# Performance work log

Measured on AMD Instinct MI355X. Metric: run time of the kernel, lower is better.

The kernel has to match this reference:

```python
import jax, jax.numpy as jnp
import numpy as np

EPS_BN = 1e-5

def _conv1x1(x, w, b):
    # x: [B,C,N], w: [O,C], b: [O] -> [B,O,N]
    return jnp.einsum('oc,bcn->bon', w, x) + b[:, None]

def _bn(x, g, b):
    # BatchNorm1d in training mode: batch stats over (B, N), biased variance
    mu = jnp.mean(x, axis=(0, 2), keepdims=True)
    var = jnp.var(x, axis=(0, 2), keepdims=True)
    return g[:, None] * (x - mu) / jnp.sqrt(var + EPS_BN) + b[:, None]

def _lrelu(x):
    return jnp.where(x >= 0, x, 0.2 * x)

def setup_inputs() -> dict:
    key = jax.random.key(0)
    B, N, S = 4, 16384, 2048
    D1, D2, FINT = 128, 256, 64
    IN, M1, M2 = D1 + D2, 256, 128
    ks = jax.random.split(key, 20)
    def rn(k, shape, scale=1.0):
        return jax.random.normal(k, shape, dtype=jnp.float32) * scale
    return {
        'xyz1': rn(ks[0], (B, 3, N)),
        'xyz2': rn(ks[1], (B, 3, S)),
        'points1': rn(ks[2], (B, D1, N)),
        'points2': rn(ks[3], (B, D2, S)),
        'conv1_w': rn(ks[4], (M1, IN), 0.05), 'conv1_b': rn(ks[5], (M1,), 0.05),
        'bn1_g': jnp.ones((M1,), jnp.float32), 'bn1_b': jnp.zeros((M1,), jnp.float32),
        'conv2_w': rn(ks[6], (M2, M1), 0.05), 'conv2_b': rn(ks[7], (M2,), 0.05),
        'bn2_g': jnp.ones((M2,), jnp.float32), 'bn2_b': jnp.zeros((M2,), jnp.float32),
        'wg_w': rn(ks[8], (FINT, D2), 0.05), 'wg_b': rn(ks[9], (FINT,), 0.05),
        'wg_bn_g': jnp.ones((FINT,), jnp.float32), 'wg_bn_b': jnp.zeros((FINT,), jnp.float32),
        'wx_w': rn(ks[10], (FINT, D1), 0.05), 'wx_b': rn(ks[11], (FINT,), 0.05),
        'wx_bn_g': jnp.ones((FINT,), jnp.float32), 'wx_bn_b': jnp.zeros((FINT,), jnp.float32),
        'psi_w': rn(ks[12], (1, FINT), 0.05), 'psi_b': rn(ks[13], (1,), 0.05),
        'psi_bn_g': jnp.ones((1,), jnp.float32), 'psi_bn_b': jnp.zeros((1,), jnp.float32),
    }

def reference(xyz1, xyz2, points1, points2,
              conv1_w, conv1_b, bn1_g, bn1_b,
              conv2_w, conv2_b, bn2_g, bn2_b,
              wg_w, wg_b, wg_bn_g, wg_bn_b,
              wx_w, wx_b, wx_bn_g, wx_bn_b,
              psi_w, psi_b, psi_bn_g, psi_bn_b):
    x1 = xyz1.transpose(0, 2, 1)        # [B,N,3]
    x2 = xyz2.transpose(0, 2, 1)        # [B,S,3]
    p2 = points2.transpose(0, 2, 1)     # [B,S,D2]
    # squared euclidean distances [B,N,S]
    d = (jnp.sum(x1 * x1, -1)[:, :, None]
         + jnp.sum(x2 * x2, -1)[:, None, :]
         - 2.0 * jnp.einsum('bnc,bsc->bns', x1, x2))
    # 3 smallest distances (torch: full sort + slice [:3])
    neg, idx = jax.lax.top_k(-d, 3)     # idx: [B,N,3]
    d3 = -neg
    recip = 1.0 / (d3 + 1e-8)
    w = recip / jnp.sum(recip, -1, keepdims=True)  # [B,N,3]
    gathered = jax.vmap(lambda p, i: p[i])(p2, idx)  # [B,N,3,D2]
    interp = jnp.einsum('bnkd,bnk->bnd', gathered, w)  # [B,N,D2]
    interp_t = interp.transpose(0, 2, 1)               # [B,D2,N]
    # attention gate: g = interpolated, x = points1
    g1 = _bn(_conv1x1(interp_t, wg_w, wg_b), wg_bn_g, wg_bn_b)
    xx1 = _bn(_conv1x1(points1, wx_w, wx_b), wx_bn_g, wx_bn_b)
    psi = jax.nn.sigmoid(_bn(_conv1x1(_lrelu(g1 + xx1), psi_w, psi_b), psi_bn_g, psi_bn_b))
    p1 = points1 * psi                                  # [B,D1,N]
    new = jnp.concatenate([p1, interp_t], axis=1)       # [B,D1+D2,N]
    new = _lrelu(_bn(_conv1x1(new, conv1_w, conv1_b), bn1_g, bn1_b))
    new = _lrelu(_bn(_conv1x1(new, conv2_w, conv2_b), bn2_g, bn2_b))
    return new
```

## Files before the change

### kernel.cpp

```cpp
#include <hip/hip_runtime.h>
#include <hip/hip_bf16.h>

#define Bq    4
#define NPTS  16384
#define SPTS  2048
#define NCH   8
#define SCH   (SPTS/NCH)
#define CNTF  65536.0f
#define BNEPS 1e-5f

typedef unsigned short u16t;
typedef unsigned int   u32t;
typedef __attribute__((ext_vector_type(8))) short s16x8;
typedef __attribute__((ext_vector_type(4))) float f32x4;

#define AS1(p) ((const __attribute__((address_space(1))) void*)(p))
#define AS3(p) ((__attribute__((address_space(3))) void*)(p))

__device__ __forceinline__ float b2f(u16t u){
  union { u32t i; float f; } v; v.i = ((u32t)u) << 16; return v.f;
}
__device__ __forceinline__ u16t f2b(float f){
  __hip_bfloat16 h = __float2bfloat16(f);
  return *reinterpret_cast<u16t*>(&h);
}
__device__ __forceinline__ float lrelu(float x){ return x >= 0.0f ? x : 0.2f*x; }

#define ST_WG  0
#define ST_WX  128
#define ST_PSI 256
#define ST_BN1 272
#define ST_BN2 784

#define WOFF_C1 0
#define WOFF_C2 98304
#define WOFF_WG 131072
#define WOFF_WX 147456
#define WTOTAL  155648

#define O_STATS  0u
#define O_WB     8192u
#define O_PSIPRE 319488u
#define O_SP     O_PSIPRE
#define O_P2T    581632u
#define O_PART   O_P2T
#define O_P1T    4775936u
#define O_INT    21553152u
#define O_H1     55107584u
#define O_PD     O_H1
#define O_PI     (O_H1 + 6291456u)
#define O_IDX3   (O_H1 + 12582912u)
#define O_W3     (O_H1 + 13369344u)
#define O_YG     O_H1
#define O_YX     (O_H1 + 8388608u)
#define O_H2     O_INT

__global__ __launch_bounds__(256) void knn_prep_kernel(const float* __restrict__ xyz2, float4* __restrict__ sp){
  int i = blockIdx.x*256 + threadIdx.x;
  int b = i >> 11, s = i & (SPTS-1);
  float x = xyz2[(b*3+0)*SPTS+s];
  float y = xyz2[(b*3+1)*SPTS+s];
  float z = xyz2[(b*3+2)*SPTS+s];
  sp[i] = make_float4(x, y, z, x*x+y*y+z*z);
}

__global__ __launch_bounds__(256) void knn_part_kernel(const float* __restrict__ xyz1, const float4* __restrict__ sp,
                                                       float* __restrict__ pd, int* __restrict__ pi){
  const int b = blockIdx.z;
  const int c = blockIdx.y;
  const int n = blockIdx.x*256 + threadIdx.x;
  const float4* cp = sp + (size_t)b*SPTS + c*SCH;
  float px = xyz1[(b*3+0)*NPTS+n];
  float py = xyz1[(b*3+1)*NPTS+n];
  float pz = xyz1[(b*3+2)*NPTS+n];
  float s1 = px*px+py*py+pz*pz;
  float d0=3.4e38f, d1=3.4e38f, d2=3.4e38f;
  int   i0=0, i1=0, i2=0;
  const int cbase = c*SCH;
  #pragma unroll 8
  for (int s=0; s<SCH; ++s){
    float4 q = cp[s];
    float dot = fmaf(pz, q.z, fmaf(py, q.y, px*q.x));
    float key = (s1 + q.w) - 2.0f*dot;
    int gi = cbase + s;
    bool c0 = key < d0, c1 = key < d1, c2 = key < d2;
    int ni2 = c1 ? i1 : (c2 ? gi : i2);
    int ni1 = c0 ? i0 : (c1 ? gi : i1);
    i0 = c0 ? gi : i0;
    float nd2 = fminf(d2, fmaxf(d1, key));
    d1 = __builtin_amdgcn_fmed3f(d0, d1, key);
    d0 = fminf(d0, key);
    d2 = nd2; i1 = ni1; i2 = ni2;
  }
  size_t base = (((size_t)b*NPTS + n)*NCH + c)*3;
  pd[base]=d0; pd[base+1]=d1; pd[base+2]=d2;
  pi[base]=i0; pi[base+1]=i1; pi[base+2]=i2;
}

__global__ __launch_bounds__(256) void knn_merge_kernel(const float* __restrict__ pd, const int* __restrict__ pi,
                                                        int* __restrict__ idx3, float* __restrict__ w3){
  const int p = blockIdx.x*256 + threadIdx.x;
  const float* dp = pd + (size_t)p*NCH*3;
  const int*   ip = pi + (size_t)p*NCH*3;
  float d0=3.4e38f, d1=3.4e38f, d2=3.4e38f;
  int   i0=0, i1=0, i2=0;
  #pragma unroll
  for (int k=0; k<NCH*3; ++k){
    float key = dp[k]; int gi = ip[k];
    bool c0 = key < d0, c1 = key < d1, c2 = key < d2;
    int ni2 = c1 ? i1 : (c2 ? gi : i2);
    int ni1 = c0 ? i0 : (c1 ? gi : i1);
    i0 = c0 ? gi : i0;
    float nd2 = fminf(d2, fmaxf(d1, key));
    d1 = __builtin_amdgcn_fmed3f(d0, d1, key);
    d0 = fminf(d0, key);
    d2 = nd2; i1 = ni1; i2 = ni2;
  }
  float r0=1.0f/(d0+1e-8f), r1=1.0f/(d1+1e-8f), r2=1.0f/(d2+1e-8f);
  float rs = r0+r1+r2;
  size_t base = (size_t)p*3;
  idx3[base]=i0; idx3[base+1]=i1; idx3[base+2]=i2;
  w3[base]=r0/rs; w3[base+1]=r1/rs; w3[base+2]=r2/rs;
}

template<int C, int NN>
__global__ __launch_bounds__(256) void tpose_kernel(const float* __restrict__ src, u16t* __restrict__ dst){
  __shared__ float tile[64][65];
  const int n0 = blockIdx.x * 64;
  const int c0 = blockIdx.y * 64;
  const int b  = blockIdx.z;
  const int t  = threadIdx.x;
  #pragma unroll
  for (int i = 0; i < 16; ++i){
    int idx = t + i*256;
    int cc = idx >> 6, nn = idx & 63;
    tile[cc][nn] = src[((size_t)b*C + c0 + cc)*NN + n0 + nn];
  }
  __syncthreads();
  #pragma unroll
  for (int i = 0; i < 16; ++i){
    int idx = t + i*256;
    int nn = idx >> 6, cc = idx & 63;
    dst[((size_t)b*NN + n0 + nn)*C + c0 + cc] = f2b(tile[cc][nn]);
  }
}

__global__ __launch_bounds__(256) void wcvt_kernel(const float* __restrict__ w1, const float* __restrict__ w2,
                                                   const float* __restrict__ wg, const float* __restrict__ wx,
                                                   u16t* __restrict__ wb){
  int i = blockIdx.x*256 + threadIdx.x;
  if (i >= WTOTAL) return;
  float v;
  if      (i < WOFF_C2) v = w1[i];
  else if (i < WOFF_WG) v = w2[i - WOFF_C2];
  else if (i < WOFF_WX) v = wg[i - WOFF_WG];
  else                  v = wx[i - WOFF_WX];
  wb[i] = f2b(v);
}

__global__ __launch_bounds__(256) void interp_kernel(const u16t* __restrict__ p2t, const int* __restrict__ idx3,
                                                     const float* __restrict__ w3, u16t* __restrict__ it){
  const int t = threadIdx.x;
  const int pid = blockIdx.x*8 + (t >> 5);
  const int l = t & 31;
  const int b = pid >> 14;
  size_t pb = (size_t)pid*3;
  int i0 = idx3[pb], i1 = idx3[pb+1], i2 = idx3[pb+2];
  float w0 = w3[pb], w1 = w3[pb+1], w2 = w3[pb+2];
  const u16t* r0 = p2t + ((size_t)b*SPTS + i0)*256 + l*8;
  const u16t* r1 = p2t + ((size_t)b*SPTS + i1)*256 + l*8;
  const u16t* r2 = p2t + ((size_t)b*SPTS + i2)*256 + l*8;
  uint4 q0 = *reinterpret_cast<const uint4*>(r0);
  uint4 q1 = *reinterpret_cast<const uint4*>(r1);
  uint4 q2 = *reinterpret_cast<const uint4*>(r2);
  const u32t* a0 = reinterpret_cast<const u32t*>(&q0);
  const u32t* a1 = reinterpret_cast<const u32t*>(&q1);
  const u32t* a2 = reinterpret_cast<const u32t*>(&q2);
  u32t ow[4];
  #pragma unroll
  for (int j = 0; j < 4; ++j){
    u32t u0 = a0[j], u1 = a1[j], u2 = a2[j];
    float lo = fmaf(w2, b2f((u16t)u2), fmaf(w1, b2f((u16t)u1), w0*b2f((u16t)u0)));
    float hi = fmaf(w2, b2f((u16t)(u2>>16)), fmaf(w1, b2f((u16t)(u1>>16)), w0*b2f((u16t)(u0>>16))));
    ow[j] = (u32t)f2b(lo) | ((u32t)f2b(hi) << 16);
  }
  *reinterpret_cast<uint4*>(it + (size_t)pid*256 + l*8) = make_uint4(ow[0], ow[1], ow[2], ow[3]);
}

template<int CIN, int OUT, bool SPLIT>
__global__ __launch_bounds__(256, 1) void mfma_conv_kernel(const u16t* __restrict__ xa, const u16t* __restrict__ xb,
                                                           const u16t* __restrict__ W, const float* __restrict__ bias,
                                                           u16t* __restrict__ y, float* __restrict__ partial,
                                                           const float* __restrict__ psipre, const float* __restrict__ stpsi,
                                                           const float* __restrict__ pbn_g, const float* __restrict__ pbn_b){
  constexpr int MW = OUT/4;
  constexpr int MF = MW/16;
  constexpr int NC = CIN/64;
  constexpr int CSTR = OUT + 8;
  constexpr int LDSZ = (CSTR*64 > 8192) ? CSTR*64 : 8192;
  __shared__ u16t lds[LDSZ];
  u16t* sbuf0 = lds;
  u16t* sbuf1 = lds + 4096;
  const int bid = blockIdx.x;
  const int b = bid >> 8;
  const int n0 = (bid & 255) * 64;
  const int wv = threadIdx.x >> 6;
  const int lane = threadIdx.x & 63;
  const int lr = lane & 15;
  const int kg = lane >> 4;
  const int m0 = wv * MW;
  const int t = threadIdx.x;

  float psiv[4];
  if (SPLIT){
    float m  = stpsi[0]*(1.0f/CNTF);
    float vv = fmaxf(stpsi[1]*(1.0f/CNTF) - m*m, 0.0f);
    float iv = 1.0f/sqrtf(vv + BNEPS);
    float ap = pbn_g[0]*iv;
    float bp = pbn_b[0] - m*ap;
    #pragma unroll
    for (int nf = 0; nf < 4; ++nf){
      float z = fmaf(psipre[b*NPTS + n0 + nf*16 + lr], ap, bp);
      psiv[nf] = 1.0f/(1.0f + expf(-z));
    }
  }

  f32x4 acc[MF][4];
  #pragma unroll
  for (int mf = 0; mf < MF; ++mf)
    #pragma unroll
    for (int nf = 0; nf < 4; ++nf){ acc[mf][nf][0]=0.f; acc[mf][nf][1]=0.f; acc[mf][nf][2]=0.f; acc[mf][nf][3]=0.f; }

  const u16t* wrow[MF];
  #pragma unroll
  for (int mf = 0; mf < MF; ++mf)
    wrow[mf] = W + (size_t)(m0 + mf*16 + lr)*CIN + kg*8;

  const int prow0 = wv*16 + (lane>>3);
  const int gslot = (lane & 7) ^ ((lane >> 3) & 7);
  int rdoff[2][4];
  #pragma unroll
  for (int ks = 0; ks < 2; ++ks)
    #pragma unroll
    for (int nf = 0; nf < 4; ++nf)
      rdoff[ks][nf] = (nf*16 + lr)*64 + (((ks*4 + kg) ^ (lr & 7)) << 3);

  auto stage = [&](int c, int buf){
    #pragma unroll
    for (int i = 0; i < 2; ++i){
      int p = prow0 + i*8;
      const u16t* g;
      if (SPLIT){
        if (c < 2) g = xa + ((size_t)b*NPTS + n0 + p)*128 + c*64     + gslot*8;
        else       g = xb + ((size_t)b*NPTS + n0 + p)*256 + (c-2)*64 + gslot*8;
      } else {
        g = xa + ((size_t)b*NPTS + n0 + p)*CIN + c*64 + gslot*8;
      }
      u16t* l = (buf ? sbuf1 : sbuf0) + (wv*16 + i*8)*64;
      __builtin_amdgcn_global_load_lds(AS1(g), AS3(l), 16, 0, 0);
    }
  };

  stage(0, 0);
  __syncthreads();
  #pragma unroll
  for (int c = 0; c < NC; ++c){
    if (c + 1 < NC) stage(c+1, (c+1)&1);
    #pragma unroll
    for (int ks = 0; ks < 2; ++ks){
      const int k0 = c*2 + ks;
      s16x8 av[MF];
      #pragma unroll
      for (int mf = 0; mf < MF; ++mf)
        av[mf] = *reinterpret_cast<const s16x8*>(wrow[mf] + k0*32);
      s16x8 bv[4];
      #pragma unroll
      for (int nf = 0; nf < 4; ++nf)
        bv[nf] = *reinterpret_cast<const s16x8*>(((c&1) ? sbuf1 : sbuf0) + rdoff[ks][nf]);
      #pragma unroll
      for (int mf = 0; mf < MF; ++mf)
        #pragma unroll
        for (int nf = 0; nf < 4; ++nf)
          acc[mf][nf] = __builtin_amdgcn_mfma_f32_16x16x32_bf16(av[mf], bv[nf], acc[mf][nf], 0, 0, 0);
    }
    if (SPLIT && c == 1){
      #pragma unroll
      for (int mf = 0; mf < MF; ++mf)
        #pragma unroll
        for (int nf = 0; nf < 4; ++nf){
          acc[mf][nf][0] *= psiv[nf]; acc[mf][nf][1] *= psiv[nf];
          acc[mf][nf][2] *= psiv[nf]; acc[mf][nf][3] *= psiv[nf];
        }
    }
    __syncthreads();
  }

  #pragma unroll
  for (int mf = 0; mf < MF; ++mf){
    int mb = m0 + mf*16 + kg*4;
    float4 bs = *reinterpret_cast<const float4*>(bias + mb);
    float s0=0.f,s1=0.f,s2=0.f,s3=0.f,q0=0.f,q1=0.f,q2=0.f,q3=0.f;
    #pragma unroll
    for (int nf = 0; nf < 4; ++nf){
      int row = nf*16 + lr;
      float v0 = acc[mf][nf][0] + bs.x;
      float v1 = acc[mf][nf][1] + bs.y;
      float v2 = acc[mf][nf][2] + bs.z;
      float v3 = acc[mf][nf][3] + bs.w;
      s0+=v0; q0+=v0*v0; s1+=v1; q1+=v1*v1;
      s2+=v2; q2+=v2*v2; s3+=v3; q3+=v3*v3;
      uint2 pv;
      pv.x = (u32t)f2b(v0) | ((u32t)f2b(v1) << 16);
      pv.y = (u32t)f2b(v2) | ((u32t)f2b(v3) << 16);
      *reinterpret_cast<uint2*>(&lds[row*CSTR + mb]) = pv;
    }
    #pragma unroll
    for (int o = 1; o < 16; o <<= 1){
      s0 += __shfl_xor(s0, o); s1 += __shfl_xor(s1, o);
      s2 += __shfl_xor(s2, o); s3 += __shfl_xor(s3, o);
      q0 += __shfl_xor(q0, o); q1 += __shfl_xor(q1, o);
      q2 += __shfl_xor(q2, o); q3 += __shfl_xor(q3, o);
    }
    if (lr == 0){
      float* pp = partial + (size_t)bid*(OUT*2) + mb*2;
      pp[0]=s0; pp[1]=q0; pp[2]=s1; pp[3]=q1;
      pp[4]=s2; pp[5]=q2; pp[6]=s3; pp[7]=q3;
    }
  }
  __syncthreads();
  constexpr int CH8 = OUT/8;
  #pragma unroll
  for (int i = 0; i < (64*CH8)/256; ++i){
    int idx = t + i*256;
    int row = idx / CH8, c8 = idx % CH8;
    uint4 v = *reinterpret_cast<const uint4*>(&lds[row*CSTR + c8*8]);
    *reinterpret_cast<uint4*>(y + ((size_t)b*NPTS + n0 + row)*OUT + c8*8) = v;
  }
}

template<int E>
__global__ __launch_bounds__(256) void reduce_stats_kernel(const float* __restrict__ p, float* __restrict__ st){
  __shared__ float ls[8][32];
  const int t = threadIdx.x;
  const int kq = t >> 5, es = t & 31;
  const int e = blockIdx.x*32 + es;
  float s = 0.f;
  const float* pp = p + (size_t)kq*128*E + e;
  #pragma unroll 16
  for (int i = 0; i < 128; ++i) s += pp[(size_t)i*E];
  ls[kq][es] = s;
  __syncthreads();
  if (kq == 0){
    st[e] = ((ls[0][es]+ls[1][es])+(ls[2][es]+ls[3][es]))
          + ((ls[4][es]+ls[5][es])+(ls[6][es]+ls[7][es]));
  }
}

__global__ __launch_bounds__(256) void gate_kernel(const u16t* __restrict__ yg, const u16t* __restrict__ yx,
                                                   const float* __restrict__ stg, const float* __restrict__ stx,
                                                   const float* __restrict__ wg_bn_g, const float* __restrict__ wg_bn_b,
                                                   const float* __restrict__ wx_bn_g, const float* __restrict__ wx_bn_b,
                                                   const float* __restrict__ psi_w, const float* __restrict__ psi_b,
                                                   float* __restrict__ psipre, float* __restrict__ stpsi){
  __shared__ float lag[64], lbg[64], lax[64], lbx[64], lpw[64];
  __shared__ float red[8];
  const int t = threadIdx.x;
  if (t < 64){
    float m  = stg[t*2] * (1.0f/CNTF);
    float vv = fmaxf(stg[t*2+1]*(1.0f/CNTF) - m*m, 0.0f);
    float iv = 1.0f/sqrtf(vv + BNEPS);
    float gm = wg_bn_g[t];
    lag[t] = gm*iv; lbg[t] = wg_bn_b[t] - m*gm*iv;
    m  = stx[t*2] * (1.0f/CNTF);
    vv = fmaxf(stx[t*2+1]*(1.0f/CNTF) - m*m, 0.0f);
    iv = 1.0f/sqrtf(vv + BNEPS);
    gm = wx_bn_g[t];
    lax[t] = gm*iv; lbx[t] = wx_bn_b[t] - m*gm*iv;
    lpw[t] = psi_w[t];
  }
  __syncthreads();
  const int p = blockIdx.x*256 + t;
  const u16t* rg = yg + (size_t)p*64;
  const u16t* rx = yx + (size_t)p*64;
  float acc = psi_b[0];
  #pragma unroll
  for (int u = 0; u < 8; ++u){
    uint4 qg = *reinterpret_cast<const uint4*>(rg + u*8);
    uint4 qx = *reinterpret_cast<const uint4*>(rx + u*8);
    const u32t* g4 = reinterpret_cast<const u32t*>(&qg);
    const u32t* x4 = reinterpret_cast<const u32t*>(&qx);
    #pragma unroll
    for (int e = 0; e < 4; ++e){
      int j = u*8 + e*2;
      float gv0 = fmaf(b2f((u16t)g4[e]),        lag[j],   lbg[j]);
      float xv0 = fmaf(b2f((u16t)x4[e]),        lax[j],   lbx[j]);
      float gv1 = fmaf(b2f((u16t)(g4[e]>>16)),  lag[j+1], lbg[j+1]);
      float xv1 = fmaf(b2f((u16t)(x4[e]>>16)),  lax[j+1], lbx[j+1]);
      acc = fmaf(lpw[j],   lrelu(gv0 + xv0), acc);
      acc = fmaf(lpw[j+1], lrelu(gv1 + xv1), acc);
    }
  }
  psipre[p] = acc;
  float s = acc, q = acc*acc;
  #pragma unroll
  for (int o = 32; o; o >>= 1){ s += __shfl_xor(s, o); q += __shfl_xor(q, o); }
  if ((t & 63) == 0){ red[(t>>6)*2] = s; red[(t>>6)*2+1] = q; }
  __syncthreads();
  if (t == 0){
    atomicAdd(&stpsi[0], red[0]+red[2]+red[4]+red[6]);
    atomicAdd(&stpsi[1], red[1]+red[3]+red[5]+red[7]);
  }
}

__global__ __launch_bounds__(256) void bnrelu256_kernel(u16t* __restrict__ x, const float* __restrict__ st,
                                                        const float* __restrict__ g, const float* __restrict__ bb){
  __shared__ float sa[256], sc[256];
  const int t = threadIdx.x;
  {
    float m  = st[t*2]*(1.0f/CNTF);
    float vv = fmaxf(st[t*2+1]*(1.0f/CNTF) - m*m, 0.0f);
    float iv = 1.0f/sqrtf(vv + BNEPS);
    float gm = g[t];
    sa[t] = gm*iv; sc[t] = bb[t] - m*gm*iv;
  }
  __syncthreads();
  size_t e4 = ((size_t)blockIdx.x*256 + t)*4;
  int c0 = (int)(e4 & 255);
  uint2 v = *reinterpret_cast<uint2*>(x + e4);
  float f0 = lrelu(fmaf(b2f((u16t)v.x),        sa[c0],   sc[c0]));
  float f1 = lrelu(fmaf(b2f((u16t)(v.x>>16)),  sa[c0+1], sc[c0+1]));
  float f2 = lrelu(fmaf(b2f((u16t)v.y),        sa[c0+2], sc[c0+2]));
  float f3 = lrelu(fmaf(b2f((u16t)(v.y>>16)),  sa[c0+3], sc[c0+3]));
  v.x = (u32t)f2b(f0) | ((u32t)f2b(f1) << 16);
  v.y = (u32t)f2b(f2) | ((u32t)f2b(f3) << 16);
  *reinterpret_cast<uint2*>(x + e4) = v;
}

__global__ __launch_bounds__(256) void final_kernel(const u16t* __restrict__ h2, const float* __restrict__ st,
                                                    const float* __restrict__ g, const float* __restrict__ bb,
                                                    float* __restrict__ out){
  __shared__ float am[128], cm[128];
  __shared__ float tile[64][129];
  const int t = threadIdx.x;
  if (t < 128){
    float m  = st[t*2]*(1.0f/CNTF);
    float vv = fmaxf(st[t*2+1]*(1.0f/CNTF) - m*m, 0.0f);
    float iv = 1.0f/sqrtf(vv + BNEPS);
    float gm = g[t];
    am[t] = gm*iv; cm[t] = bb[t] - m*gm*iv;
  }
  __syncthreads();
  const int n0 = blockIdx.x * 64;
  const int b  = blockIdx.y;
  #pragma unroll
  for (int i = 0; i < 32; ++i){
    int idx = t + i*256;
    int mm = idx & 127, nn = idx >> 7;
    float v = fmaf(b2f(h2[((size_t)b*NPTS + n0 + nn)*128 + mm]), am[mm], cm[mm]);
    tile[nn][mm] = lrelu(v);
  }
  __syncthreads();
  #pragma unroll
  for (int i = 0; i < 32; ++i){
    int idx = t + i*256;
    int nn = idx & 63, mm = idx >> 6;
    out[((size_t)(b*128 + mm))*NPTS + n0 + nn] = tile[nn][mm];
  }
}

extern "C" void kernel_launch(void* const* d_in, const int* in_sizes, int n_in,
                              void* d_out, int out_size, void* d_ws, size_t ws_size,
                              hipStream_t stream){
  const float* xyz1    = (const float*)d_in[0];
  const float* xyz2    = (const float*)d_in[1];
  const float* points1 = (const float*)d_in[2];
  const float* points2 = (const float*)d_in[3];
  const float* conv1_w = (const float*)d_in[4];
  const float* conv1_b = (const float*)d_in[5];
  const float* bn1_g   = (const float*)d_in[6];
  const float* bn1_b   = (const float*)d_in[7];
  const float* conv2_w = (const float*)d_in[8];
  const float* conv2_b = (const float*)d_in[9];
  const float* bn2_g   = (const float*)d_in[10];
  const float* bn2_b   = (const float*)d_in[11];
  const float* wg_w    = (const float*)d_in[12];
  const float* wg_b    = (const float*)d_in[13];
  const float* wg_bn_g = (const float*)d_in[14];
  const float* wg_bn_b = (const float*)d_in[15];
  const float* wx_w    = (const float*)d_in[16];
  const float* wx_b    = (const float*)d_in[17];
  const float* wx_bn_g = (const float*)d_in[18];
  const float* wx_bn_b = (const float*)d_in[19];
  const float* psi_w   = (const float*)d_in[20];
  const float* psi_b   = (const float*)d_in[21];
  const float* psi_bn_g= (const float*)d_in[22];
  const float* psi_bn_b= (const float*)d_in[23];

  char* ws = (char*)d_ws;
  float* stats  = (float*)(ws + O_STATS);
  u16t*  wb     = (u16t*)(ws + O_WB);
  float* psipre = (float*)(ws + O_PSIPRE);
  float4* sp    = (float4*)(ws + O_SP);
  u16t*  p2t    = (u16t*)(ws + O_P2T);
  float* part   = (float*)(ws + O_PART);
  u16t*  p1t    = (u16t*)(ws + O_P1T);
  u16t*  itp    = (u16t*)(ws + O_INT);
  u16t*  h1t    = (u16t*)(ws + O_H1);
  float* pd     = (float*)(ws + O_PD);
  int*   pi     = (int*)(ws + O_PI);
  int*   idx3   = (int*)(ws + O_IDX3);
  float* w3     = (float*)(ws + O_W3);
  u16t*  ygt    = (u16t*)(ws + O_YG);
  u16t*  yxt    = (u16t*)(ws + O_YX);
  u16t*  h2t    = (u16t*)(ws + O_H2);

  hipMemsetAsync(ws + O_STATS, 0, 8192, stream);

  knn_prep_kernel<<<(Bq*SPTS)/256, 256, 0, stream>>>(xyz2, sp);
  knn_part_kernel<<<dim3(NPTS/256, NCH, Bq), 256, 0, stream>>>(xyz1, sp, pd, pi);
  knn_merge_kernel<<<(Bq*NPTS)/256, 256, 0, stream>>>(pd, pi, idx3, w3);
  tpose_kernel<256, SPTS><<<dim3(SPTS/64, 4, Bq), 256, 0, stream>>>(points2, p2t);
  interp_kernel<<<(Bq*NPTS)/8, 256, 0, stream>>>(p2t, idx3, w3, itp);
  tpose_kernel<128, NPTS><<<dim3(NPTS/64, 2, Bq), 256, 0, stream>>>(points1, p1t);
  wcvt_kernel<<<(WTOTAL+255)/256, 256, 0, stream>>>(conv1_w, conv2_w, wg_w, wx_w, wb);

  mfma_conv_kernel<256, 64, false><<<Bq*(NPTS/64), 256, 0, stream>>>(itp, nullptr, wb+WOFF_WG, wg_b, ygt, part,
                                                                     nullptr, nullptr, nullptr, nullptr);
  reduce_stats_kernel<128><<<4, 256, 0, stream>>>(part, stats+ST_WG);
  mfma_conv_kernel<128, 64, false><<<Bq*(NPTS/64), 256, 0, stream>>>(p1t, nullptr, wb+WOFF_WX, wx_b, yxt, part,
                                                                     nullptr, nullptr, nullptr, nullptr);
  reduce_stats_kernel<128><<<4, 256, 0, stream>>>(part, stats+ST_WX);
  gate_kernel<<<256, 256, 0, stream>>>(ygt, yxt, stats+ST_WG, stats+ST_WX,
                                       wg_bn_g, wg_bn_b, wx_bn_g, wx_bn_b,
                                       psi_w, psi_b, psipre, stats+ST_PSI);

  mfma_conv_kernel<384, 256, true><<<Bq*(NPTS/64), 256, 0, stream>>>(p1t, itp, wb+WOFF_C1, conv1_b, h1t, part,
                                                                     psipre, stats+ST_PSI, psi_bn_g, psi_bn_b);
  reduce_stats_kernel<512><<<16, 256, 0, stream>>>(part, stats+ST_BN1);
  bnrelu256_kernel<<<16384, 256, 0, stream>>>(h1t, stats+ST_BN1, bn1_g, bn1_b);

  mfma_conv_kernel<256, 128, false><<<Bq*(NPTS/64), 256, 0, stream>>>(h1t, nullptr, wb+WOFF_C2, conv2_b, h2t, part,
                                                                      nullptr, nullptr, nullptr, nullptr);
  reduce_stats_kernel<256><<<8, 256, 0, stream>>>(part, stats+ST_BN2);
  final_kernel<<<dim3(NPTS/64, Bq), 256, 0, stream>>>(h2t, stats+ST_BN2, bn2_g, bn2_b, (float*)d_out);
}
```

Measured before the change: 224.2 us.

## Double MFMA conv point tile to 128 per block to reuse weight fragments

Each conv block now covers 128 points instead of 64. Every weight fragment loaded from global memory is reused across 8 MFMA column tiles instead of 4, and the grid is halved. The epilogue stores the two 64-row halves through LDS in turn, and the stats reduction now reads half as many partials. Holding twice the accumulator registers per wave cuts occupancy headroom, and the 512-block grid gives fewer blocks per CU on a 256-CU part.

Result: faster. 212.5 us (-5.2%).

```diff
diff --git a/kernel.cpp b/kernel.cpp
--- a/kernel.cpp
+++ b/kernel.cpp
@@ -197,13 +197,11 @@
   constexpr int MF = MW/16;
   constexpr int NC = CIN/64;
   constexpr int CSTR = OUT + 8;
-  constexpr int LDSZ = (CSTR*64 > 8192) ? CSTR*64 : 8192;
-  __shared__ u16t lds[LDSZ];
-  u16t* sbuf0 = lds;
-  u16t* sbuf1 = lds + 4096;
+  constexpr int LDSE = (64*CSTR > 16384) ? 64*CSTR : 16384;
+  __shared__ u16t lds[LDSE];
   const int bid = blockIdx.x;
-  const int b = bid >> 8;
-  const int n0 = (bid & 255) * 64;
+  const int b = bid >> 7;
+  const int n0 = (bid & 127) * 128;
   const int wv = threadIdx.x >> 6;
   const int lane = threadIdx.x & 63;
   const int lr = lane & 15;
@@ -211,7 +209,7 @@
   const int m0 = wv * MW;
   const int t = threadIdx.x;
 
-  float psiv[4];
+  float psiv[8];
   if (SPLIT){
     float m  = stpsi[0]*(1.0f/CNTF);
     float vv = fmaxf(stpsi[1]*(1.0f/CNTF) - m*m, 0.0f);
@@ -219,35 +217,35 @@
     float ap = pbn_g[0]*iv;
     float bp = pbn_b[0] - m*ap;
     #pragma unroll
-    for (int nf = 0; nf < 4; ++nf){
+    for (int nf = 0; nf < 8; ++nf){
       float z = fmaf(psipre[b*NPTS + n0 + nf*16 + lr], ap, bp);
       psiv[nf] = 1.0f/(1.0f + expf(-z));
     }
   }
 
-  f32x4 acc[MF][4];
+  f32x4 acc[MF][8];
   #pragma unroll
   for (int mf = 0; mf < MF; ++mf)
     #pragma unroll
-    for (int nf = 0; nf < 4; ++nf){ acc[mf][nf][0]=0.f; acc[mf][nf][1]=0.f; acc[mf][nf][2]=0.f; acc[mf][nf][3]=0.f; }
+    for (int nf = 0; nf < 8; ++nf){ acc[mf][nf][0]=0.f; acc[mf][nf][1]=0.f; acc[mf][nf][2]=0.f; acc[mf][nf][3]=0.f; }
 
   const u16t* wrow[MF];
   #pragma unroll
   for (int mf = 0; mf < MF; ++mf)
     wrow[mf] = W + (size_t)(m0 + mf*16 + lr)*CIN + kg*8;
 
-  const int prow0 = wv*16 + (lane>>3);
+  const int prow0 = wv*32 + (lane>>3);
   const int gslot = (lane & 7) ^ ((lane >> 3) & 7);
-  int rdoff[2][4];
+  int rdoff[2][8];
   #pragma unroll
   for (int ks = 0; ks < 2; ++ks)
     #pragma unroll
-    for (int nf = 0; nf < 4; ++nf)
+    for (int nf = 0; nf < 8; ++nf)
       rdoff[ks][nf] = (nf*16 + lr)*64 + (((ks*4 + kg) ^ (lr & 7)) << 3);
 
   auto stage = [&](int c, int buf){
     #pragma unroll
-    for (int i = 0; i < 2; ++i){
+    for (int i = 0; i < 4; ++i){
       int p = prow0 + i*8;
       const u16t* g;
       if (SPLIT){
@@ -256,7 +254,7 @@
       } else {
         g = xa + ((size_t)b*NPTS + n0 + p)*CIN + c*64 + gslot*8;
       }
-      u16t* l = (buf ? sbuf1 : sbuf0) + (wv*16 + i*8)*64;
+      u16t* l = lds + buf*8192 + (wv*32 + i*8)*64;
       __builtin_amdgcn_global_load_lds(AS1(g), AS3(l), 16, 0, 0);
     }
   };
@@ -273,21 +271,24 @@
       #pragma unroll
       for (int mf = 0; mf < MF; ++mf)
         av[mf] = *reinterpret_cast<const s16x8*>(wrow[mf] + k0*32);
-      s16x8 bv[4];
       #pragma unroll
-      for (int nf = 0; nf < 4; ++nf)
-        bv[nf] = *reinterpret_cast<const s16x8*>(((c&1) ? sbuf1 : sbuf0) + rdoff[ks][nf]);
-      #pragma unroll
-      for (int mf = 0; mf < MF; ++mf)
+      for (int h = 0; h < 2; ++h){
+        s16x8 bv[4];
         #pragma unroll
-        for (int nf = 0; nf < 4; ++nf)
-          acc[mf][nf] = __builtin_amdgcn_mfma_f32_16x16x32_bf16(av[mf], bv[nf], acc[mf][nf], 0, 0, 0);
+        for (int j = 0; j < 4; ++j)
+          bv[j] = *reinterpret_cast<const s16x8*>(lds + (c&1)*8192 + rdoff[ks][h*4+j]);
+        #pragma unroll
+        for (int mf = 0; mf < MF; ++mf)
+          #pragma unroll
+          for (int j = 0; j < 4; ++j)
+            acc[mf][h*4+j] = __builtin_amdgcn_mfma_f32_16x16x32_bf16(av[mf], bv[j], acc[mf][h*4+j], 0, 0, 0);
+      }
     }
     if (SPLIT && c == 1){
       #pragma unroll
       for (int mf = 0; mf < MF; ++mf)
         #pragma unroll
-        for (int nf = 0; nf < 4; ++nf){
+        for (int nf = 0; nf < 8; ++nf){
           acc[mf][nf][0] *= psiv[nf]; acc[mf][nf][1] *= psiv[nf];
           acc[mf][nf][2] *= psiv[nf]; acc[mf][nf][3] *= psiv[nf];
         }
@@ -301,18 +302,14 @@
     float4 bs = *reinterpret_cast<const float4*>(bias + mb);
     float s0=0.f,s1=0.f,s2=0.f,s3=0.f,q0=0.f,q1=0.f,q2=0.f,q3=0.f;
     #pragma unroll
-    for (int nf = 0; nf < 4; ++nf){
-      int row = nf*16 + lr;
+    for (int nf = 0; nf < 8; ++nf){
       float v0 = acc[mf][nf][0] + bs.x;
       float v1 = acc[mf][nf][1] + bs.y;
       float v2 = acc[mf][nf][2] + bs.z;
       float v3 = acc[mf][nf][3] + bs.w;
+      acc[mf][nf][0]=v0; acc[mf][nf][1]=v1; acc[mf][nf][2]=v2; acc[mf][nf][3]=v3;
       s0+=v0; q0+=v0*v0; s1+=v1; q1+=v1*v1;
       s2+=v2; q2+=v2*v2; s3+=v3; q3+=v3*v3;
-      uint2 pv;
-      pv.x = (u32t)f2b(v0) | ((u32t)f2b(v1) << 16);
-      pv.y = (u32t)f2b(v2) | ((u32t)f2b(v3) << 16);
-      *reinterpret_cast<uint2*>(&lds[row*CSTR + mb]) = pv;
     }
     #pragma unroll
     for (int o = 1; o < 16; o <<= 1){
@@ -327,14 +324,32 @@
       pp[4]=s2; pp[5]=q2; pp[6]=s3; pp[7]=q3;
     }
   }
-  __syncthreads();
+
   constexpr int CH8 = OUT/8;
   #pragma unroll
-  for (int i = 0; i < (64*CH8)/256; ++i){
-    int idx = t + i*256;
-    int row = idx / CH8, c8 = idx % CH8;
-    uint4 v = *reinterpret_cast<const uint4*>(&lds[row*CSTR + c8*8]);
-    *reinterpret_cast<uint4*>(y + ((size_t)b*NPTS + n0 + row)*OUT + c8*8) = v;
+  for (int h = 0; h < 2; ++h){
+    __syncthreads();
+    #pragma unroll
+    for (int mf = 0; mf < MF; ++mf){
+      int mb = m0 + mf*16 + kg*4;
+      #pragma unroll
+      for (int j = 0; j < 4; ++j){
+        int row = j*16 + lr;
+        f32x4 v = acc[mf][h*4+j];
+        uint2 pv;
+        pv.x = (u32t)f2b(v[0]) | ((u32t)f2b(v[1]) << 16);
+        pv.y = (u32t)f2b(v[2]) | ((u32t)f2b(v[3]) << 16);
+        *reinterpret_cast<uint2*>(&lds[row*CSTR + mb]) = pv;
+      }
+    }
+    __syncthreads();
+    #pragma unroll
+    for (int i = 0; i < (64*CH8)/256; ++i){
+      int idx = t + i*256;
+      int row = idx / CH8, c8 = idx % CH8;
+      uint4 v = *reinterpret_cast<const uint4*>(&lds[row*CSTR + c8*8]);
+      *reinterpret_cast<uint4*>(y + ((size_t)b*NPTS + n0 + h*64 + row)*OUT + c8*8) = v;
+    }
   }
 }
 
@@ -345,9 +360,9 @@
   const int kq = t >> 5, es = t & 31;
   const int e = blockIdx.x*32 + es;
   float s = 0.f;
-  const float* pp = p + (size_t)kq*128*E + e;
+  const float* pp = p + (size_t)kq*64*E + e;
   #pragma unroll 16
-  for (int i = 0; i < 128; ++i) s += pp[(size_t)i*E];
+  for (int i = 0; i < 64; ++i) s += pp[(size_t)i*E];
   ls[kq][es] = s;
   __syncthreads();
   if (kq == 0){
@@ -524,23 +539,23 @@
   tpose_kernel<128, NPTS><<<dim3(NPTS/64, 2, Bq), 256, 0, stream>>>(points1, p1t);
   wcvt_kernel<<<(WTOTAL+255)/256, 256, 0, stream>>>(conv1_w, conv2_w, wg_w, wx_w, wb);
 
-  mfma_conv_kernel<256, 64, false><<<Bq*(NPTS/64), 256, 0, stream>>>(itp, nullptr, wb+WOFF_WG, wg_b, ygt, part,
-                                                                     nullptr, nullptr, nullptr, nullptr);
+  mfma_conv_kernel<256, 64, false><<<Bq*(NPTS/128), 256, 0, stream>>>(itp, nullptr, wb+WOFF_WG, wg_b, ygt, part,
+                                                                      nullptr, nullptr, nullptr, nullptr);
   reduce_stats_kernel<128><<<4, 256, 0, stream>>>(part, stats+ST_WG);
-  mfma_conv_kernel<128, 64, false><<<Bq*(NPTS/64), 256, 0, stream>>>(p1t, nullptr, wb+WOFF_WX, wx_b, yxt, part,
-                                                                     nullptr, nullptr, nullptr, nullptr);
+  mfma_conv_kernel<128, 64, false><<<Bq*(NPTS/128), 256, 0, stream>>>(p1t, nullptr, wb+WOFF_WX, wx_b, yxt, part,
+                                                                      nullptr, nullptr, nullptr, nullptr);
   reduce_stats_kernel<128><<<4, 256, 0, stream>>>(part, stats+ST_WX);
   gate_kernel<<<256, 256, 0, stream>>>(ygt, yxt, stats+ST_WG, stats+ST_WX,
                                        wg_bn_g, wg_bn_b, wx_bn_g, wx_bn_b,
                                        psi_w, psi_b, psipre, stats+ST_PSI);
 
-  mfma_conv_kernel<384, 256, true><<<Bq*(NPTS/64), 256, 0, stream>>>(p1t, itp, wb+WOFF_C1, conv1_b, h1t, part,
-                                                                     psipre, stats+ST_PSI, psi_bn_g, psi_bn_b);
+  mfma_conv_kernel<384, 256, true><<<Bq*(NPTS/128), 256, 0, stream>>>(p1t, itp, wb+WOFF_C1, conv1_b, h1t, part,
+                                                                      psipre, stats+ST_PSI, psi_bn_g, psi_bn_b);
   reduce_stats_kernel<512><<<16, 256, 0, stream>>>(part, stats+ST_BN1);
   bnrelu256_kernel<<<16384, 256, 0, stream>>>(h1t, stats+ST_BN1, bn1_g, bn1_b);
 
-  mfma_conv_kernel<256, 128, false><<<Bq*(NPTS/64), 256, 0, stream>>>(h1t, nullptr, wb+WOFF_C2, conv2_b, h2t, part,
-                                                                      nullptr, nullptr, nullptr, nullptr);
+  mfma_conv_kernel<256, 128, false><<<Bq*(NPTS/128), 256, 0, stream>>>(h1t, nullptr, wb+WOFF_C2, conv2_b, h2t, part,
+                                                                       nullptr, nullptr, nullptr, nullptr);
   reduce_stats_kernel<256><<<8, 256, 0, stream>>>(part, stats+ST_BN2);
   final_kernel<<<dim3(NPTS/64, Bq), 256, 0, stream>>>(h2t, stats+ST_BN2, bn2_g, bn2_b, (float*)d_out);
 }
```
